# Kernel tuning notes

Hardware: AMD Instinct MI355X
Metric: run time of the kernel (lower is better)

Reference implementation:

```python
import jax, jax.numpy as jnp
import numpy as np
import math

B, T, E, H = 4, 1024, 1024, 16
D = E // H  # head_dim = 64
EPS = 1e-5


def setup_inputs() -> dict:
    key = jax.random.key(0)
    k1, k2, k3 = jax.random.split(key, 3)
    x = jax.random.normal(k1, (B, T, E), dtype=jnp.float32)
    scale = jnp.ones((E,), dtype=jnp.float32)
    w_qkv = jax.random.normal(k2, (3 * E, E), dtype=jnp.float32) * (1.0 / math.sqrt(E))
    w_proj = jax.random.normal(k3, (E, E), dtype=jnp.float32) * (1.0 / math.sqrt(E))
    return {"x": x, "scale": scale, "w_qkv": w_qkv, "w_proj": w_proj}


def reference(x, scale, w_qkv, w_proj):
    # RMSNorm
    xn = x * jax.lax.rsqrt(jnp.mean(x * x, axis=-1, keepdims=True) + EPS) * scale
    # QKV projection (torch Linear: y = x @ W.T)
    qkv = jnp.einsum('bte,fe->btf', xn, w_qkv)  # [B,T,3E]
    q, k, v = jnp.split(qkv, 3, axis=-1)
    # [B,T,E] -> [B,H,T,D]
    q = q.reshape(B, T, H, D).transpose(0, 2, 1, 3)
    k = k.reshape(B, T, H, D).transpose(0, 2, 1, 3)
    v = v.reshape(B, T, H, D).transpose(0, 2, 1, 3)
    # causal attention
    attn = jnp.einsum('bhqd,bhkd->bhqk', q, k) / math.sqrt(D)
    causal = jnp.tril(jnp.ones((T, T), dtype=bool))
    attn = jnp.where(causal, attn, -jnp.inf)
    attn = jax.nn.softmax(attn, axis=-1)
    out = jnp.einsum('bhqk,bhkd->bhqd', attn, v)  # [B,H,T,D]
    out = out.transpose(0, 2, 1, 3).reshape(B, T, E)
    # output projection
    return jnp.einsum('bte,fe->btf', out, w_proj)
```

## Files before the change

kernel.cpp:

```cpp
#include <hip/hip_runtime.h>
#include <hip/hip_bf16.h>
#include <stdint.h>

#define B_SZ 4
#define T_SEQ 1024
#define E_DIM 1024
#define NH 16
#define HD 64
#define THREE_E 3072
#define NTOK 4096

typedef unsigned short u16;
typedef unsigned int u32;
using short8v = __attribute__((ext_vector_type(8))) short;
using short4v = __attribute__((ext_vector_type(4))) short;
using f32x4 = __attribute__((ext_vector_type(4))) float;

__device__ __forceinline__ u16 f2bf(float f) {
    union { float f; uint32_t u; } c; c.f = f;
    uint32_t u = c.u;
    uint32_t r = (u + 0x7FFFu + ((u >> 16) & 1u)) >> 16;
    return (u16)r;
}

__device__ __forceinline__ u32 cvt_pk_bf16(float lo, float hi) {
    u32 r;
    asm("v_cvt_pk_bf16_f32 %0, %1, %2" : "=v"(r) : "v"(lo), "v"(hi));
    return r;
}

__device__ __forceinline__ void gload_lds16(const u16* g, u16* l) {
    __builtin_amdgcn_global_load_lds((const __attribute__((address_space(1))) void*)g,
                                     (__attribute__((address_space(3))) void*)l, 16, 0, 0);
}

__global__ __launch_bounds__(256) void prep_kernel(const float* __restrict__ x,
                                                   const float* __restrict__ scale,
                                                   const float* __restrict__ wq,
                                                   const float* __restrict__ wp,
                                                   u16* __restrict__ xn,
                                                   u16* __restrict__ wqb,
                                                   u16* __restrict__ wpb) {
    int bx = blockIdx.x;
    int tid = threadIdx.x;
    if (bx < 4096) {
        int row = bx;
        const float4* xr = reinterpret_cast<const float4*>(x + (size_t)row * E_DIM);
        float4 v = xr[tid];
        float ss = v.x * v.x + v.y * v.y + v.z * v.z + v.w * v.w;
        for (int off = 32; off > 0; off >>= 1) ss += __shfl_xor(ss, off);
        __shared__ float red[4];
        if ((tid & 63) == 0) red[tid >> 6] = ss;
        __syncthreads();
        float total = red[0] + red[1] + red[2] + red[3];
        float rs = rsqrtf(total * (1.0f / E_DIM) + 1e-5f);
        float4 s = reinterpret_cast<const float4*>(scale)[tid];
        u16* o = xn + (size_t)row * E_DIM + tid * 4;
        o[0] = f2bf(v.x * rs * s.x);
        o[1] = f2bf(v.y * rs * s.y);
        o[2] = f2bf(v.z * rs * s.z);
        o[3] = f2bf(v.w * rs * s.w);
    } else {
        const int NQ = (THREE_E * E_DIM) / 4;
        const int NP = (E_DIM * E_DIM) / 4;
        int i = (bx - 4096) * 256 + tid;
        if (i < NQ) {
            float4 v = reinterpret_cast<const float4*>(wq)[i];
            u16* o = wqb + (size_t)i * 4;
            o[0] = f2bf(v.x); o[1] = f2bf(v.y); o[2] = f2bf(v.z); o[3] = f2bf(v.w);
        } else if (i < NQ + NP) {
            int j = i - NQ;
            float4 v = reinterpret_cast<const float4*>(wp)[j];
            u16* o = wpb + (size_t)j * 4;
            o[0] = f2bf(v.x); o[1] = f2bf(v.y); o[2] = f2bf(v.z); o[3] = f2bf(v.w);
        }
    }
}

template <int BN, bool OUT_BF16>
__global__ __launch_bounds__(256) void gemm_lds_kernel(const u16* __restrict__ A,
                                                       const u16* __restrict__ Bw,
                                                       void* __restrict__ C,
                                                       int N, int K) {
    constexpr int NFR = BN / 32;
    __shared__ u16 As[128 * 64];
    __shared__ u16 Bs[BN * 64];
    int tid = threadIdx.x;
    int lane = tid & 63, wid = tid >> 6;
    int lq = lane & 15, lg = lane >> 4;

    int gx = gridDim.x;
    int nwg = gx * gridDim.y;
    int orig = blockIdx.y * gx + blockIdx.x;
    int cpx = nwg >> 3;
    int swz = (orig & 7) * cpx + (orig >> 3);
    int bx = swz % gx, by = swz / gx;
    int mblk = by * 128, nblk = bx * BN;

    int srowA = wid * 32 + (lane >> 3);
    int srowB = wid * (BN / 4) + (lane >> 3);
    int csw = ((lane & 7) ^ ((lane >> 3) & 7)) * 8;
    const u16* gA = A + (size_t)(mblk + srowA) * K + csw;
    const u16* gB = Bw + (size_t)(nblk + srowB) * K + csw;
    u16* lA = As + wid * 2048;
    u16* lB = Bs + wid * (BN / 4) * 64;

    f32x4 acc[4][NFR] = {};
    int m0w = (wid >> 1) * 64;
    int n0w = (wid & 1) * (BN / 2);
    int r7 = lq & 7;
    const int NT = K / 64;

#pragma unroll
    for (int i = 0; i < 4; ++i) gload_lds16(gA + (size_t)i * 8 * K, lA + i * 512);
#pragma unroll
    for (int i = 0; i < NFR; ++i) gload_lds16(gB + (size_t)i * 8 * K, lB + i * 512);

    for (int t = 0; t < NT; ++t) {
        __syncthreads();
        short8v af[2][4], bf[2][NFR];
#pragma unroll
        for (int kk = 0; kk < 2; ++kk) {
#pragma unroll
            for (int mi = 0; mi < 4; ++mi)
                af[kk][mi] = *reinterpret_cast<const short8v*>(
                    &As[(m0w + mi * 16 + lq) * 64 + ((kk * 4 + lg) ^ r7) * 8]);
#pragma unroll
            for (int ni = 0; ni < NFR; ++ni)
                bf[kk][ni] = *reinterpret_cast<const short8v*>(
                    &Bs[(n0w + ni * 16 + lq) * 64 + ((kk * 4 + lg) ^ r7) * 8]);
        }
        __syncthreads();
        if (t + 1 < NT) {
            int k0 = (t + 1) * 64;
#pragma unroll
            for (int i = 0; i < 4; ++i) gload_lds16(gA + k0 + (size_t)i * 8 * K, lA + i * 512);
#pragma unroll
            for (int i = 0; i < NFR; ++i) gload_lds16(gB + k0 + (size_t)i * 8 * K, lB + i * 512);
        }
        __builtin_amdgcn_sched_barrier(0);
        __builtin_amdgcn_s_setprio(1);
#pragma unroll
        for (int mi = 0; mi < 4; ++mi)
#pragma unroll
            for (int ni = 0; ni < NFR; ++ni) {
                acc[mi][ni] = __builtin_amdgcn_mfma_f32_16x16x32_bf16(af[0][mi], bf[0][ni], acc[mi][ni], 0, 0, 0);
                acc[mi][ni] = __builtin_amdgcn_mfma_f32_16x16x32_bf16(af[1][mi], bf[1][ni], acc[mi][ni], 0, 0, 0);
            }
        __builtin_amdgcn_s_setprio(0);
    }
#pragma unroll
    for (int mi = 0; mi < 4; ++mi) {
#pragma unroll
        for (int ni = 0; ni < NFR; ++ni) {
#pragma unroll
            for (int j = 0; j < 4; ++j) {
                int row = mblk + m0w + mi * 16 + lg * 4 + j;
                int col = nblk + n0w + ni * 16 + lq;
                float val = acc[mi][ni][j];
                if (OUT_BF16)
                    ((u16*)C)[(size_t)row * N + col] = f2bf(val);
                else
                    ((float*)C)[(size_t)row * N + col] = val;
            }
        }
    }
}

template <bool DIAG>
__device__ __forceinline__ void attn_tile(const u16 (*__restrict__ Kt)[72],
                                          const u16 (*__restrict__ Vt)[72],
                                          const short8v* __restrict__ qf,
                                          f32x4* __restrict__ o,
                                          float& l_r,
                                          int lq, int lg, int w4, int kt64, int qg) {
    const float CLOG = 0.18033688011112042f;
    const float MOFF = 11.541560327111707f;
    int ksmax = DIAG ? w4 : 3;
    f32x4 st[4] = {};
    __builtin_amdgcn_s_setprio(1);
#pragma unroll
    for (int ks = 0; ks < 4; ++ks) {
        if (ks <= ksmax) {
            short8v a0 = *reinterpret_cast<const short8v*>(&Kt[ks * 16 + lq][lg * 8]);
            short8v a1 = *reinterpret_cast<const short8v*>(&Kt[ks * 16 + lq][32 + lg * 8]);
            st[ks] = __builtin_amdgcn_mfma_f32_16x16x32_bf16(a0, qf[0], st[ks], 0, 0, 0);
            st[ks] = __builtin_amdgcn_mfma_f32_16x16x32_bf16(a1, qf[1], st[ks], 0, 0, 0);
        }
    }
    __builtin_amdgcn_s_setprio(0);
    float p[4][4];
    float psum = 0.f;
#pragma unroll
    for (int ks = 0; ks < 4; ++ks)
#pragma unroll
        for (int j = 0; j < 4; ++j) {
            float v = st[ks][j];
            if (DIAG) {
                int kg = kt64 + ks * 16 + lg * 4 + j;
                v = (ks <= ksmax && kg <= qg) ? v : -INFINITY;
            }
            float pv = exp2f(fmaf(v, CLOG, -MOFF));
            p[ks][j] = pv;
            psum += pv;
        }
    l_r += psum;
    union { u32 w2[2]; short4v v; } pa[4];
#pragma unroll
    for (int ks = 0; ks < 4; ++ks) {
        pa[ks].w2[0] = cvt_pk_bf16(p[ks][0], p[ks][1]);
        pa[ks].w2[1] = cvt_pk_bf16(p[ks][2], p[ks][3]);
    }
    __builtin_amdgcn_s_setprio(1);
#pragma unroll
    for (int ni = 0; ni < 4; ++ni) {
        int d = ni * 16 + lq;
        int sw = ((d >> 3) & 7) << 3;
        const u16* vrow = Vt[d];
#pragma unroll
        for (int ks = 0; ks < 4; ++ks) {
            if (ks <= ksmax) {
                short4v vb = *reinterpret_cast<const short4v*>(&vrow[(ks * 16 + lg * 4) ^ sw]);
                o[ni] = __builtin_amdgcn_mfma_f32_16x16x16bf16_1k(pa[ks].v, vb, o[ni], 0, 0, 0);
            }
        }
    }
    __builtin_amdgcn_s_setprio(0);
}

__global__ __launch_bounds__(512) void attn_kernel(const u16* __restrict__ qkv,
                                                   u16* __restrict__ out) {
    int tid = threadIdx.x;
    int lane = tid & 63, wid = tid >> 6;
    int lq = lane & 15, lg = lane >> 4;
    int w4 = wid & 3;
    bool is_hi = wid >= 4;
    int bh = blockIdx.y;
    int b = bh >> 4, h = bh & 15;
    int qlo_blk = blockIdx.x;
    int qhi_blk = 15 - qlo_blk;
    int myblk = is_hi ? qhi_blk : qlo_blk;
    int qt = myblk * 64 + w4 * 16;

    const u16* base = qkv + (size_t)b * T_SEQ * THREE_E;
    const u16* Qb = base + h * HD;
    const u16* Kb = base + E_DIM + h * HD;

    __shared__ __align__(16) u16 Kt[2][64][72];
    __shared__ __align__(16) u16 Vt[2][64][72];

    short8v qf[2];
    {
        const u16* qr = Qb + (size_t)(qt + lq) * THREE_E + lg * 8;
        qf[0] = *reinterpret_cast<const short8v*>(qr);
        qf[1] = *reinterpret_cast<const short8v*>(qr + 32);
    }
    f32x4 o[4] = {};
    float l_r = 0.f;
    int qg = qt + lq;

    int row_s = tid >> 3, c8 = tid & 7;
    short8v kreg, vreg;

    {
        const u16* src = Kb + (size_t)row_s * THREE_E + c8 * 8;
        kreg = *reinterpret_cast<const short8v*>(src);
        vreg = *reinterpret_cast<const short8v*>(src + E_DIM);
    }
    {
        *reinterpret_cast<short8v*>(&Kt[0][row_s][c8 * 8]) = kreg;
        int rs = row_s ^ (c8 << 3);
#pragma unroll
        for (int e = 0; e < 8; ++e) Vt[0][c8 * 8 + e][rs] = (u16)vreg[e];
    }
    if (qhi_blk >= 1) {
        const u16* src = Kb + (size_t)(64 + row_s) * THREE_E + c8 * 8;
        kreg = *reinterpret_cast<const short8v*>(src);
        vreg = *reinterpret_cast<const short8v*>(src + E_DIM);
    }
    __syncthreads();

    for (int kt = 0; kt <= qhi_blk; ++kt) {
        int cur = kt & 1;
        if (kt < qhi_blk) {
            *reinterpret_cast<short8v*>(&Kt[cur ^ 1][row_s][c8 * 8]) = kreg;
            int rs = row_s ^ (c8 << 3);
#pragma unroll
            for (int e = 0; e < 8; ++e) Vt[cur ^ 1][c8 * 8 + e][rs] = (u16)vreg[e];
            if (kt + 1 < qhi_blk) {
                const u16* src = Kb + (size_t)((kt + 2) * 64 + row_s) * THREE_E + c8 * 8;
                kreg = *reinterpret_cast<const short8v*>(src);
                vreg = *reinterpret_cast<const short8v*>(src + E_DIM);
            }
        }
        if (is_hi) {
            if (kt < qhi_blk)
                attn_tile<false>(Kt[cur], Vt[cur], qf, o, l_r, lq, lg, w4, kt * 64, qg);
            else
                attn_tile<true>(Kt[cur], Vt[cur], qf, o, l_r, lq, lg, w4, kt * 64, qg);
        } else {
            if (kt < qlo_blk)
                attn_tile<false>(Kt[cur], Vt[cur], qf, o, l_r, lq, lg, w4, kt * 64, qg);
            else if (kt == qlo_blk)
                attn_tile<true>(Kt[cur], Vt[cur], qf, o, l_r, lq, lg, w4, kt * 64, qg);
        }
        __syncthreads();
    }
    float lf = l_r;
    lf += __shfl_xor(lf, 16); lf += __shfl_xor(lf, 32);
#pragma unroll
    for (int j = 0; j < 4; ++j) {
        float linv = 1.0f / __shfl(lf, lg * 4 + j);
        size_t row = (size_t)b * T_SEQ + qt + lg * 4 + j;
#pragma unroll
        for (int ni = 0; ni < 4; ++ni)
            out[row * E_DIM + h * HD + ni * 16 + lq] = f2bf(o[ni][j] * linv);
    }
}

extern "C" void kernel_launch(void* const* d_in, const int* in_sizes, int n_in,
                              void* d_out, int out_size, void* d_ws, size_t ws_size,
                              hipStream_t stream) {
    const float* x = (const float*)d_in[0];
    const float* scale = (const float*)d_in[1];
    const float* w_qkv = (const float*)d_in[2];
    const float* w_proj = (const float*)d_in[3];
    float* out = (float*)d_out;

    char* ws = (char*)d_ws;
    u16* xn   = (u16*)(ws);
    u16* wqb  = (u16*)(ws + (8ull << 20));
    u16* wpb  = (u16*)(ws + (14ull << 20));
    u16* qkv  = (u16*)(ws + (16ull << 20));
    u16* aout = (u16*)(ws + (40ull << 20));

    prep_kernel<<<dim3(8192), dim3(256), 0, stream>>>(x, scale, w_qkv, w_proj, xn, wqb, wpb);
    gemm_lds_kernel<128, true><<<dim3(THREE_E / 128, NTOK / 128), dim3(256), 0, stream>>>(
        xn, wqb, (void*)qkv, THREE_E, E_DIM);
    attn_kernel<<<dim3(8, B_SZ * NH), dim3(512), 0, stream>>>(qkv, aout);
    gemm_lds_kernel<64, false><<<dim3(E_DIM / 64, NTOK / 128), dim3(256), 0, stream>>>(
        aout, wpb, (void*)out, E_DIM, E_DIM);
}
```

Measured before the change: 86.56 us.

## Switch attention to 32x32x16 MFMA tiles with four query blocks per workgroup

Rewrites the attention inner tile to use 32x32x16 bf16 MFMAs. Each wave now owns 32 query rows, and the score-to-PV operand layout is rearranged with permlane32_swap. The grid is halved: each 512-thread block now covers four query blocks (two low, two high) sharing one K/V stream, and K in LDS gets an XOR swizzle for the new read pattern. The aim is to cut MFMA instruction count and K/V LDS/global reloads per query, at the cost of fewer workgroups (256) and coarser causal masking granularity.

```diff
diff --git a/kernel.cpp b/kernel.cpp
--- a/kernel.cpp
+++ b/kernel.cpp
@@ -13,8 +13,9 @@
 typedef unsigned short u16;
 typedef unsigned int u32;
 using short8v = __attribute__((ext_vector_type(8))) short;
-using short4v = __attribute__((ext_vector_type(4))) short;
 using f32x4 = __attribute__((ext_vector_type(4))) float;
+using f32x16 = __attribute__((ext_vector_type(16))) float;
+using uint2v = __attribute__((ext_vector_type(2))) unsigned int;
 
 __device__ __forceinline__ u16 f2bf(float f) {
     union { float f; uint32_t u; } c; c.f = f;
@@ -167,80 +168,107 @@
     }
 }
 
+#define PACK_KS(SRC, S1, OUT)                                                   \
+    do {                                                                        \
+        u32 P00 = cvt_pk_bf16((SRC)[8 * (S1) + 0], (SRC)[8 * (S1) + 1]);        \
+        u32 P01 = cvt_pk_bf16((SRC)[8 * (S1) + 2], (SRC)[8 * (S1) + 3]);        \
+        u32 P10 = cvt_pk_bf16((SRC)[8 * (S1) + 4], (SRC)[8 * (S1) + 5]);        \
+        u32 P11 = cvt_pk_bf16((SRC)[8 * (S1) + 6], (SRC)[8 * (S1) + 7]);        \
+        uint2v r0 = __builtin_amdgcn_permlane32_swap(P00, P10, false, false);   \
+        uint2v r1 = __builtin_amdgcn_permlane32_swap(P01, P11, false, false);   \
+        union { u32 w[4]; short8v v; } u_;                                      \
+        u_.w[0] = r0[0]; u_.w[1] = r1[0]; u_.w[2] = r0[1]; u_.w[3] = r1[1];     \
+        OUT = u_.v;                                                             \
+    } while (0)
+
 template <bool DIAG>
-__device__ __forceinline__ void attn_tile(const u16 (*__restrict__ Kt)[72],
-                                          const u16 (*__restrict__ Vt)[72],
-                                          const short8v* __restrict__ qf,
-                                          f32x4* __restrict__ o,
-                                          float& l_r,
-                                          int lq, int lg, int w4, int kt64, int qg) {
+__device__ __forceinline__ void attn_tile32(const u16 (*__restrict__ Kt)[72],
+                                            const u16 (*__restrict__ Vt)[72],
+                                            const short8v* __restrict__ qf,
+                                            f32x16* __restrict__ o2,
+                                            float& l_r,
+                                            int l32, int lhi, int kt64, int qg, int qtop) {
     const float CLOG = 0.18033688011112042f;
     const float MOFF = 11.541560327111707f;
-    int ksmax = DIAG ? w4 : 3;
-    f32x4 st[4] = {};
-    __builtin_amdgcn_s_setprio(1);
-#pragma unroll
-    for (int ks = 0; ks < 4; ++ks) {
-        if (ks <= ksmax) {
-            short8v a0 = *reinterpret_cast<const short8v*>(&Kt[ks * 16 + lq][lg * 8]);
-            short8v a1 = *reinterpret_cast<const short8v*>(&Kt[ks * 16 + lq][32 + lg * 8]);
-            st[ks] = __builtin_amdgcn_mfma_f32_16x16x32_bf16(a0, qf[0], st[ks], 0, 0, 0);
-            st[ks] = __builtin_amdgcn_mfma_f32_16x16x32_bf16(a1, qf[1], st[ks], 0, 0, 0);
-        }
-    }
-    __builtin_amdgcn_s_setprio(0);
-    float p[4][4];
+    f32x16 st0 = 0.f, st1 = 0.f;
+    {
+        int row = l32;
+        int rx = row & 7;
+        __builtin_amdgcn_s_setprio(1);
+#pragma unroll
+        for (int ds = 0; ds < 4; ++ds) {
+            short8v kf = *reinterpret_cast<const short8v*>(
+                &Kt[row][(((ds << 1) | lhi) ^ rx) << 3]);
+            st0 = __builtin_amdgcn_mfma_f32_32x32x16_bf16(kf, qf[ds], st0, 0, 0, 0);
+        }
+        __builtin_amdgcn_s_setprio(0);
+    }
+    if (!DIAG || (kt64 + 32 <= qtop)) {
+        int row = 32 + l32;
+        int rx = row & 7;
+        __builtin_amdgcn_s_setprio(1);
+#pragma unroll
+        for (int ds = 0; ds < 4; ++ds) {
+            short8v kf = *reinterpret_cast<const short8v*>(
+                &Kt[row][(((ds << 1) | lhi) ^ rx) << 3]);
+            st1 = __builtin_amdgcn_mfma_f32_32x32x16_bf16(kf, qf[ds], st1, 0, 0, 0);
+        }
+        __builtin_amdgcn_s_setprio(0);
+    }
     float psum = 0.f;
 #pragma unroll
-    for (int ks = 0; ks < 4; ++ks)
-#pragma unroll
-        for (int j = 0; j < 4; ++j) {
-            float v = st[ks][j];
-            if (DIAG) {
-                int kg = kt64 + ks * 16 + lg * 4 + j;
-                v = (ks <= ksmax && kg <= qg) ? v : -INFINITY;
+    for (int r = 0; r < 16; ++r) {
+        float v0 = st0[r], v1 = st1[r];
+        if (DIAG) {
+            int krel = (r & 3) + ((r >> 2) << 3) + (lhi << 2);
+            v0 = (kt64 + krel <= qg) ? v0 : -INFINITY;
+            v1 = (kt64 + 32 + krel <= qg) ? v1 : -INFINITY;
+        }
+        float p0 = exp2f(fmaf(v0, CLOG, -MOFF));
+        float p1 = exp2f(fmaf(v1, CLOG, -MOFF));
+        st0[r] = p0; st1[r] = p1;
+        psum += p0 + p1;
+    }
+    l_r += psum;
+    short8v paf[4];
+    PACK_KS(st0, 0, paf[0]);
+    PACK_KS(st0, 1, paf[1]);
+    PACK_KS(st1, 0, paf[2]);
+    PACK_KS(st1, 1, paf[3]);
+#pragma unroll
+    for (int db = 0; db < 2; ++db) {
+        int d = db * 32 + l32;
+        const u16* vrow = Vt[d];
+        int dx = (d >> 3) & 7;
+        __builtin_amdgcn_s_setprio(1);
+#pragma unroll
+        for (int ks = 0; ks < 4; ++ks) {
+            if (!DIAG || (kt64 + ks * 16 <= qtop)) {
+                short8v vf = *reinterpret_cast<const short8v*>(
+                    &vrow[(((ks << 1) | lhi) ^ dx) << 3]);
+                o2[db] = __builtin_amdgcn_mfma_f32_32x32x16_bf16(paf[ks], vf, o2[db], 0, 0, 0);
             }
-            float pv = exp2f(fmaf(v, CLOG, -MOFF));
-            p[ks][j] = pv;
-            psum += pv;
-        }
-    l_r += psum;
-    union { u32 w2[2]; short4v v; } pa[4];
-#pragma unroll
-    for (int ks = 0; ks < 4; ++ks) {
-        pa[ks].w2[0] = cvt_pk_bf16(p[ks][0], p[ks][1]);
-        pa[ks].w2[1] = cvt_pk_bf16(p[ks][2], p[ks][3]);
-    }
-    __builtin_amdgcn_s_setprio(1);
-#pragma unroll
-    for (int ni = 0; ni < 4; ++ni) {
-        int d = ni * 16 + lq;
-        int sw = ((d >> 3) & 7) << 3;
-        const u16* vrow = Vt[d];
-#pragma unroll
-        for (int ks = 0; ks < 4; ++ks) {
-            if (ks <= ksmax) {
-                short4v vb = *reinterpret_cast<const short4v*>(&vrow[(ks * 16 + lg * 4) ^ sw]);
-                o[ni] = __builtin_amdgcn_mfma_f32_16x16x16bf16_1k(pa[ks].v, vb, o[ni], 0, 0, 0);
-            }
-        }
-    }
-    __builtin_amdgcn_s_setprio(0);
+        }
+        __builtin_amdgcn_s_setprio(0);
+    }
 }
 
 __global__ __launch_bounds__(512) void attn_kernel(const u16* __restrict__ qkv,
                                                    u16* __restrict__ out) {
     int tid = threadIdx.x;
     int lane = tid & 63, wid = tid >> 6;
-    int lq = lane & 15, lg = lane >> 4;
-    int w4 = wid & 3;
-    bool is_hi = wid >= 4;
+    int l32 = lane & 31, lhi = lane >> 5;
+    int bx = blockIdx.x;
     int bh = blockIdx.y;
     int b = bh >> 4, h = bh & 15;
-    int qlo_blk = blockIdx.x;
-    int qhi_blk = 15 - qlo_blk;
-    int myblk = is_hi ? qhi_blk : qlo_blk;
-    int qt = myblk * 64 + w4 * 16;
+    int pa = (wid >> 2) & 1;
+    int ishi = (wid >> 1) & 1;
+    int s = wid & 1;
+    int qblk = ishi ? (pa ? 14 - 2 * bx : 15 - 2 * bx)
+                    : (pa ? 2 * bx + 1 : 2 * bx);
+    int ktmax = 15 - 2 * bx;
+    int qt = qblk * 64 + s * 32;
+    int qg = qt + l32, qtop = qt + 31;
 
     const u16* base = qkv + (size_t)b * T_SEQ * THREE_E;
     const u16* Qb = base + h * HD;
@@ -249,15 +277,16 @@
     __shared__ __align__(16) u16 Kt[2][64][72];
     __shared__ __align__(16) u16 Vt[2][64][72];
 
-    short8v qf[2];
+    short8v qf[4];
     {
-        const u16* qr = Qb + (size_t)(qt + lq) * THREE_E + lg * 8;
-        qf[0] = *reinterpret_cast<const short8v*>(qr);
-        qf[1] = *reinterpret_cast<const short8v*>(qr + 32);
-    }
-    f32x4 o[4] = {};
+        const u16* qr = Qb + (size_t)(qt + l32) * THREE_E + lhi * 8;
+#pragma unroll
+        for (int ds = 0; ds < 4; ++ds)
+            qf[ds] = *reinterpret_cast<const short8v*>(qr + ds * 16);
+    }
+    f32x16 o2[2];
+    o2[0] = 0.f; o2[1] = 0.f;
     float l_r = 0.f;
-    int qg = qt + lq;
 
     int row_s = tid >> 3, c8 = tid & 7;
     short8v kreg, vreg;
@@ -268,53 +297,46 @@
         vreg = *reinterpret_cast<const short8v*>(src + E_DIM);
     }
     {
-        *reinterpret_cast<short8v*>(&Kt[0][row_s][c8 * 8]) = kreg;
+        *reinterpret_cast<short8v*>(&Kt[0][row_s][((c8 ^ (row_s & 7)) << 3)]) = kreg;
         int rs = row_s ^ (c8 << 3);
 #pragma unroll
         for (int e = 0; e < 8; ++e) Vt[0][c8 * 8 + e][rs] = (u16)vreg[e];
     }
-    if (qhi_blk >= 1) {
+    if (ktmax >= 1) {
         const u16* src = Kb + (size_t)(64 + row_s) * THREE_E + c8 * 8;
         kreg = *reinterpret_cast<const short8v*>(src);
         vreg = *reinterpret_cast<const short8v*>(src + E_DIM);
     }
     __syncthreads();
 
-    for (int kt = 0; kt <= qhi_blk; ++kt) {
+    for (int kt = 0; kt <= ktmax; ++kt) {
         int cur = kt & 1;
-        if (kt < qhi_blk) {
-            *reinterpret_cast<short8v*>(&Kt[cur ^ 1][row_s][c8 * 8]) = kreg;
+        if (kt < ktmax) {
+            *reinterpret_cast<short8v*>(&Kt[cur ^ 1][row_s][((c8 ^ (row_s & 7)) << 3)]) = kreg;
             int rs = row_s ^ (c8 << 3);
 #pragma unroll
             for (int e = 0; e < 8; ++e) Vt[cur ^ 1][c8 * 8 + e][rs] = (u16)vreg[e];
-            if (kt + 1 < qhi_blk) {
+            if (kt + 1 < ktmax) {
                 const u16* src = Kb + (size_t)((kt + 2) * 64 + row_s) * THREE_E + c8 * 8;
                 kreg = *reinterpret_cast<const short8v*>(src);
                 vreg = *reinterpret_cast<const short8v*>(src + E_DIM);
             }
         }
-        if (is_hi) {
-            if (kt < qhi_blk)
-                attn_tile<false>(Kt[cur], Vt[cur], qf, o, l_r, lq, lg, w4, kt * 64, qg);
-            else
-                attn_tile<true>(Kt[cur], Vt[cur], qf, o, l_r, lq, lg, w4, kt * 64, qg);
-        } else {
-            if (kt < qlo_blk)
-                attn_tile<false>(Kt[cur], Vt[cur], qf, o, l_r, lq, lg, w4, kt * 64, qg);
-            else if (kt == qlo_blk)
-                attn_tile<true>(Kt[cur], Vt[cur], qf, o, l_r, lq, lg, w4, kt * 64, qg);
-        }
+        if (kt < qblk)
+            attn_tile32<false>(Kt[cur], Vt[cur], qf, o2, l_r, l32, lhi, kt * 64, qg, qtop);
+        else if (kt == qblk)
+            attn_tile32<true>(Kt[cur], Vt[cur], qf, o2, l_r, l32, lhi, kt * 64, qg, qtop);
         __syncthreads();
     }
-    float lf = l_r;
-    lf += __shfl_xor(lf, 16); lf += __shfl_xor(lf, 32);
-#pragma unroll
-    for (int j = 0; j < 4; ++j) {
-        float linv = 1.0f / __shfl(lf, lg * 4 + j);
-        size_t row = (size_t)b * T_SEQ + qt + lg * 4 + j;
-#pragma unroll
-        for (int ni = 0; ni < 4; ++ni)
-            out[row * E_DIM + h * HD + ni * 16 + lq] = f2bf(o[ni][j] * linv);
+    float lf = l_r + __shfl_xor(l_r, 32);
+#pragma unroll
+    for (int j = 0; j < 16; ++j) {
+        int crow = (j & 3) + ((j >> 2) << 3) + (lhi << 2);
+        float linv = 1.0f / __shfl(lf, crow);
+        size_t row = (size_t)b * T_SEQ + qt + crow;
+#pragma unroll
+        for (int db = 0; db < 2; ++db)
+            out[row * E_DIM + h * HD + db * 32 + l32] = f2bf(o2[db][j] * linv);
     }
 }
 
@@ -337,7 +359,7 @@
     prep_kernel<<<dim3(8192), dim3(256), 0, stream>>>(x, scale, w_qkv, w_proj, xn, wqb, wpb);
     gemm_lds_kernel<128, true><<<dim3(THREE_E / 128, NTOK / 128), dim3(256), 0, stream>>>(
         xn, wqb, (void*)qkv, THREE_E, E_DIM);
-    attn_kernel<<<dim3(8, B_SZ * NH), dim3(512), 0, stream>>>(qkv, aout);
+    attn_kernel<<<dim3(4, B_SZ * NH), dim3(512), 0, stream>>>(qkv, aout);
     gemm_lds_kernel<64, false><<<dim3(E_DIM / 64, NTOK / 128), dim3(256), 0, stream>>>(
         aout, wpb, (void*)out, E_DIM, E_DIM);
 }
```

New measurement: 93.93 us. +8.5%, slower.

## Split paired-block attention CTAs into one q-block per 256-thread CTA

Applied to the files above, without the earlier changes.

Replaces the 512-thread attention CTA that paired a low and a high query block (sharing K/V tiles) with 256-thread CTAs that each handle a single 64-row query block. Blocks are launched heaviest-first (reversed blockIdx) to balance the causal workload. This removes wasted waits where low-block waves idle while the CTA keeps loading tiles for the high block, but it loses the K/V tile sharing between the pair and doubles K/V global traffic for low blocks.

```diff
diff --git a/kernel.cpp b/kernel.cpp
--- a/kernel.cpp
+++ b/kernel.cpp
@@ -228,19 +228,15 @@
     __builtin_amdgcn_s_setprio(0);
 }
 
-__global__ __launch_bounds__(512) void attn_kernel(const u16* __restrict__ qkv,
+__global__ __launch_bounds__(256) void attn_kernel(const u16* __restrict__ qkv,
                                                    u16* __restrict__ out) {
     int tid = threadIdx.x;
     int lane = tid & 63, wid = tid >> 6;
     int lq = lane & 15, lg = lane >> 4;
-    int w4 = wid & 3;
-    bool is_hi = wid >= 4;
     int bh = blockIdx.y;
     int b = bh >> 4, h = bh & 15;
-    int qlo_blk = blockIdx.x;
-    int qhi_blk = 15 - qlo_blk;
-    int myblk = is_hi ? qhi_blk : qlo_blk;
-    int qt = myblk * 64 + w4 * 16;
+    int qblk = (int)gridDim.x - 1 - (int)blockIdx.x;
+    int qt = qblk * 64 + wid * 16;
 
     const u16* base = qkv + (size_t)b * T_SEQ * THREE_E;
     const u16* Qb = base + h * HD;
@@ -259,51 +255,57 @@
     float l_r = 0.f;
     int qg = qt + lq;
 
-    int row_s = tid >> 3, c8 = tid & 7;
-    short8v kreg, vreg;
-
-    {
-        const u16* src = Kb + (size_t)row_s * THREE_E + c8 * 8;
-        kreg = *reinterpret_cast<const short8v*>(src);
-        vreg = *reinterpret_cast<const short8v*>(src + E_DIM);
-    }
-    {
-        *reinterpret_cast<short8v*>(&Kt[0][row_s][c8 * 8]) = kreg;
-        int rs = row_s ^ (c8 << 3);
-#pragma unroll
-        for (int e = 0; e < 8; ++e) Vt[0][c8 * 8 + e][rs] = (u16)vreg[e];
-    }
-    if (qhi_blk >= 1) {
-        const u16* src = Kb + (size_t)(64 + row_s) * THREE_E + c8 * 8;
-        kreg = *reinterpret_cast<const short8v*>(src);
-        vreg = *reinterpret_cast<const short8v*>(src + E_DIM);
+    int row_s = tid >> 2, cc = (tid & 3) * 2;
+    short8v kreg[2], vreg[2];
+
+#pragma unroll
+    for (int i = 0; i < 2; ++i) {
+        const u16* src = Kb + (size_t)row_s * THREE_E + (cc + i) * 8;
+        kreg[i] = *reinterpret_cast<const short8v*>(src);
+        vreg[i] = *reinterpret_cast<const short8v*>(src + E_DIM);
+    }
+#pragma unroll
+    for (int i = 0; i < 2; ++i) {
+        int dc = cc + i;
+        *reinterpret_cast<short8v*>(&Kt[0][row_s][dc * 8]) = kreg[i];
+        int rs = row_s ^ (dc << 3);
+#pragma unroll
+        for (int e = 0; e < 8; ++e) Vt[0][dc * 8 + e][rs] = (u16)vreg[i][e];
+    }
+    if (qblk >= 1) {
+#pragma unroll
+        for (int i = 0; i < 2; ++i) {
+            const u16* src = Kb + (size_t)(64 + row_s) * THREE_E + (cc + i) * 8;
+            kreg[i] = *reinterpret_cast<const short8v*>(src);
+            vreg[i] = *reinterpret_cast<const short8v*>(src + E_DIM);
+        }
     }
     __syncthreads();
 
-    for (int kt = 0; kt <= qhi_blk; ++kt) {
+    for (int kt = 0; kt <= qblk; ++kt) {
         int cur = kt & 1;
-        if (kt < qhi_blk) {
-            *reinterpret_cast<short8v*>(&Kt[cur ^ 1][row_s][c8 * 8]) = kreg;
-            int rs = row_s ^ (c8 << 3);
-#pragma unroll
-            for (int e = 0; e < 8; ++e) Vt[cur ^ 1][c8 * 8 + e][rs] = (u16)vreg[e];
-            if (kt + 1 < qhi_blk) {
-                const u16* src = Kb + (size_t)((kt + 2) * 64 + row_s) * THREE_E + c8 * 8;
-                kreg = *reinterpret_cast<const short8v*>(src);
-                vreg = *reinterpret_cast<const short8v*>(src + E_DIM);
-            }
-        }
-        if (is_hi) {
-            if (kt < qhi_blk)
-                attn_tile<false>(Kt[cur], Vt[cur], qf, o, l_r, lq, lg, w4, kt * 64, qg);
-            else
-                attn_tile<true>(Kt[cur], Vt[cur], qf, o, l_r, lq, lg, w4, kt * 64, qg);
-        } else {
-            if (kt < qlo_blk)
-                attn_tile<false>(Kt[cur], Vt[cur], qf, o, l_r, lq, lg, w4, kt * 64, qg);
-            else if (kt == qlo_blk)
-                attn_tile<true>(Kt[cur], Vt[cur], qf, o, l_r, lq, lg, w4, kt * 64, qg);
-        }
+        if (kt < qblk) {
+#pragma unroll
+            for (int i = 0; i < 2; ++i) {
+                int dc = cc + i;
+                *reinterpret_cast<short8v*>(&Kt[cur ^ 1][row_s][dc * 8]) = kreg[i];
+                int rs = row_s ^ (dc << 3);
+#pragma unroll
+                for (int e = 0; e < 8; ++e) Vt[cur ^ 1][dc * 8 + e][rs] = (u16)vreg[i][e];
+            }
+            if (kt + 1 < qblk) {
+#pragma unroll
+                for (int i = 0; i < 2; ++i) {
+                    const u16* src = Kb + (size_t)((kt + 2) * 64 + row_s) * THREE_E + (cc + i) * 8;
+                    kreg[i] = *reinterpret_cast<const short8v*>(src);
+                    vreg[i] = *reinterpret_cast<const short8v*>(src + E_DIM);
+                }
+            }
+        }
+        if (kt < qblk)
+            attn_tile<false>(Kt[cur], Vt[cur], qf, o, l_r, lq, lg, wid, kt * 64, qg);
+        else
+            attn_tile<true>(Kt[cur], Vt[cur], qf, o, l_r, lq, lg, wid, kt * 64, qg);
         __syncthreads();
     }
     float lf = l_r;
@@ -337,7 +339,7 @@
     prep_kernel<<<dim3(8192), dim3(256), 0, stream>>>(x, scale, w_qkv, w_proj, xn, wqb, wpb);
     gemm_lds_kernel<128, true><<<dim3(THREE_E / 128, NTOK / 128), dim3(256), 0, stream>>>(
         xn, wqb, (void*)qkv, THREE_E, E_DIM);
-    attn_kernel<<<dim3(8, B_SZ * NH), dim3(512), 0, stream>>>(qkv, aout);
+    attn_kernel<<<dim3(16, B_SZ * NH), dim3(256), 0, stream>>>(qkv, aout);
     gemm_lds_kernel<64, false><<<dim3(E_DIM / 64, NTOK / 128), dim3(256), 0, stream>>>(
         aout, wpb, (void*)out, E_DIM, E_DIM);
 }
```

New measurement: 100.3 us. 15.9% more time.

## Use 256x256-tile 8-wave ping-pong GEMM for QKV projection

Applied to the files above, without the earlier changes.

Replaces the QKV projection GEMM with a new 512-thread kernel using 256x256 output tiles, double-buffered LDS with direct global-to-LDS loads, and a barrier-synchronized interleave of LDS reads, prefetches and MFMA clusters with raised priority. The aim is to raise data reuse per tile and overlap memory traffic with matrix math. The large tile cuts the grid to 192 workgroups, which may leave some CUs idle, and the heavy LDS use limits occupancy.

```diff
diff --git a/kernel.cpp b/kernel.cpp
--- a/kernel.cpp
+++ b/kernel.cpp
@@ -77,6 +77,148 @@
     }
 }
 
+#define SYNC_MFMA16(AV, BV, MO)                                                 \
+    do {                                                                        \
+        __builtin_amdgcn_s_barrier();                                           \
+        asm volatile("s_waitcnt lgkmcnt(0)" ::: "memory");                      \
+        __builtin_amdgcn_sched_barrier(0);                                      \
+        __builtin_amdgcn_s_setprio(1);                                          \
+        _Pragma("unroll") for (int mi_ = 0; mi_ < 4; ++mi_)                     \
+            _Pragma("unroll") for (int ni_ = 0; ni_ < 4; ++ni_)                 \
+                acc[(MO) + mi_][ni_] = __builtin_amdgcn_mfma_f32_16x16x32_bf16( \
+                    (AV)[mi_], (BV)[ni_], acc[(MO) + mi_][ni_], 0, 0, 0);       \
+        __builtin_amdgcn_s_setprio(0);                                          \
+        __builtin_amdgcn_s_barrier();                                           \
+    } while (0)
+
+template <int K>
+__global__ __launch_bounds__(512, 2) void gemm8p_kernel(const u16* __restrict__ A,
+                                                        const u16* __restrict__ Bw,
+                                                        u16* __restrict__ C, int N) {
+    constexpr int NITER = K / 128;
+    __shared__ u16 As[2][16384];
+    __shared__ u16 Bs[2][16384];
+    int tid = threadIdx.x;
+    int lane = tid & 63, wid = tid >> 6;
+    int lq = lane & 15, lg = lane >> 4;
+    int wm = wid >> 2, wn = wid & 3;
+
+    int gx = gridDim.x;
+    int nwg = gx * gridDim.y;
+    int orig = blockIdx.y * gx + blockIdx.x;
+    int cpx = nwg >> 3;
+    int swz = (orig & 7) * cpx + (orig >> 3);
+    int bx = swz % gx, by = swz / gx;
+    int mblk = by * 256, nblk = bx * 256;
+
+    int srow = tid >> 3;
+    int csw = ((tid & 7) ^ (srow & 7)) * 8;
+    const u16* gA = A + (size_t)(mblk + srow) * K + csw;
+    const u16* gB = Bw + (size_t)(nblk + srow) * K + csw;
+    int dst = tid * 8;
+
+#define STG_A(t, h)                                                                  \
+    do {                                                                             \
+        _Pragma("unroll") for (int j_ = 0; j_ < 2; ++j_)                             \
+            gload_lds16(gA + (size_t)((h) * 128 + j_ * 64) * K + (t) * 64,           \
+                        &As[(t) & 1][(h) * 8192 + j_ * 4096 + dst]);                 \
+    } while (0)
+#define STG_B(t, h)                                                                  \
+    do {                                                                             \
+        _Pragma("unroll") for (int j_ = 0; j_ < 2; ++j_)                             \
+            gload_lds16(gB + (size_t)((h) * 128 + j_ * 64) * K + (t) * 64,           \
+                        &Bs[(t) & 1][(h) * 8192 + j_ * 4096 + dst]);                 \
+    } while (0)
+
+    int r7 = lq & 7;
+    int arow = wm * 128 + lq;
+    int brow = wn * 64 + lq;
+    int c0 = ((0 + lg) ^ r7) * 8;
+    int c1 = ((4 + lg) ^ r7) * 8;
+
+    f32x4 acc[8][4] = {};
+
+    STG_A(0, 0); STG_A(0, 1); STG_B(0, 0); STG_B(0, 1); STG_B(1, 0); STG_B(1, 1);
+    asm volatile("s_waitcnt vmcnt(0)" ::: "memory");
+    __builtin_amdgcn_s_barrier();
+
+    for (int i = 0; i < NITER; ++i) {
+        int t0 = 2 * i, t1 = 2 * i + 1;
+        const u16* Ab0 = As[0];
+        const u16* Bb0 = Bs[0];
+        const u16* Ab1 = As[1];
+        const u16* Bb1 = Bs[1];
+        bool pre = (i < NITER - 1);
+        short8v a[4], b0[4], b1[4];
+#pragma unroll
+        for (int mi = 0; mi < 4; ++mi)
+            a[mi] = *reinterpret_cast<const short8v*>(Ab0 + (arow + mi * 16) * 64 + c0);
+#pragma unroll
+        for (int ni = 0; ni < 4; ++ni)
+            b0[ni] = *reinterpret_cast<const short8v*>(Bb0 + (brow + ni * 16) * 64 + c0);
+        STG_A(t1, 0);
+        SYNC_MFMA16(a, b0, 0);
+#pragma unroll
+        for (int mi = 0; mi < 4; ++mi)
+            a[mi] = *reinterpret_cast<const short8v*>(Ab0 + (arow + mi * 16) * 64 + c1);
+#pragma unroll
+        for (int ni = 0; ni < 4; ++ni)
+            b1[ni] = *reinterpret_cast<const short8v*>(Bb0 + (brow + ni * 16) * 64 + c1);
+        STG_A(t1, 1);
+        SYNC_MFMA16(a, b1, 0);
+#pragma unroll
+        for (int mi = 0; mi < 4; ++mi)
+            a[mi] = *reinterpret_cast<const short8v*>(Ab0 + (arow + 64 + mi * 16) * 64 + c0);
+        if (pre) STG_B(t0 + 2, 0);
+        SYNC_MFMA16(a, b0, 4);
+#pragma unroll
+        for (int mi = 0; mi < 4; ++mi)
+            a[mi] = *reinterpret_cast<const short8v*>(Ab0 + (arow + 64 + mi * 16) * 64 + c1);
+        if (pre) STG_B(t0 + 2, 1);
+        SYNC_MFMA16(a, b1, 4);
+        if (pre) asm volatile("s_waitcnt vmcnt(4)" ::: "memory");
+        else     asm volatile("s_waitcnt vmcnt(0)" ::: "memory");
+#pragma unroll
+        for (int mi = 0; mi < 4; ++mi)
+            a[mi] = *reinterpret_cast<const short8v*>(Ab1 + (arow + mi * 16) * 64 + c0);
+#pragma unroll
+        for (int ni = 0; ni < 4; ++ni)
+            b0[ni] = *reinterpret_cast<const short8v*>(Bb1 + (brow + ni * 16) * 64 + c0);
+        if (pre) STG_A(t0 + 2, 0);
+        SYNC_MFMA16(a, b0, 0);
+#pragma unroll
+        for (int mi = 0; mi < 4; ++mi)
+            a[mi] = *reinterpret_cast<const short8v*>(Ab1 + (arow + mi * 16) * 64 + c1);
+#pragma unroll
+        for (int ni = 0; ni < 4; ++ni)
+            b1[ni] = *reinterpret_cast<const short8v*>(Bb1 + (brow + ni * 16) * 64 + c1);
+        if (pre) STG_A(t0 + 2, 1);
+        SYNC_MFMA16(a, b1, 0);
+#pragma unroll
+        for (int mi = 0; mi < 4; ++mi)
+            a[mi] = *reinterpret_cast<const short8v*>(Ab1 + (arow + 64 + mi * 16) * 64 + c0);
+        if (pre) STG_B(t1 + 2, 0);
+        SYNC_MFMA16(a, b0, 4);
+#pragma unroll
+        for (int mi = 0; mi < 4; ++mi)
+            a[mi] = *reinterpret_cast<const short8v*>(Ab1 + (arow + 64 + mi * 16) * 64 + c1);
+        if (pre) STG_B(t1 + 2, 1);
+        SYNC_MFMA16(a, b1, 4);
+        if (pre) asm volatile("s_waitcnt vmcnt(4)" ::: "memory");
+        else     asm volatile("s_waitcnt vmcnt(0)" ::: "memory");
+    }
+#pragma unroll
+    for (int mi = 0; mi < 8; ++mi)
+#pragma unroll
+        for (int ni = 0; ni < 4; ++ni)
+#pragma unroll
+            for (int j = 0; j < 4; ++j) {
+                int row = mblk + wm * 128 + mi * 16 + lg * 4 + j;
+                int col = nblk + wn * 64 + ni * 16 + lq;
+                C[(size_t)row * N + col] = f2bf(acc[mi][ni][j]);
+            }
+}
+
 template <int BN, bool OUT_BF16>
 __global__ __launch_bounds__(256) void gemm_lds_kernel(const u16* __restrict__ A,
                                                        const u16* __restrict__ Bw,
@@ -335,8 +477,8 @@
     u16* aout = (u16*)(ws + (40ull << 20));
 
     prep_kernel<<<dim3(8192), dim3(256), 0, stream>>>(x, scale, w_qkv, w_proj, xn, wqb, wpb);
-    gemm_lds_kernel<128, true><<<dim3(THREE_E / 128, NTOK / 128), dim3(256), 0, stream>>>(
-        xn, wqb, (void*)qkv, THREE_E, E_DIM);
+    gemm8p_kernel<E_DIM><<<dim3(THREE_E / 256, NTOK / 256), dim3(512), 0, stream>>>(
+        xn, wqb, qkv, THREE_E);
     attn_kernel<<<dim3(8, B_SZ * NH), dim3(512), 0, stream>>>(qkv, aout);
     gemm_lds_kernel<64, false><<<dim3(E_DIM / 64, NTOK / 128), dim3(256), 0, stream>>>(
         aout, wpb, (void*)out, E_DIM, E_DIM);
```

Result: slower. 94.58 us (+9.3%).
